# Performance work log

Hardware: AMD Instinct MI355X
Metric: run time of the kernel (lower is better)

The kernel has to match this reference:

```python
import jax, jax.numpy as jnp
import numpy as np

B, T, D_MODEL, N_HEADS, HEAD = 2, 2048, 1024, 16, 64
ROPE_BASE = 10000.0
EPS = 1e-5


def _layer_norm(x, g, b):
    m = jnp.mean(x, axis=-1, keepdims=True)
    v = jnp.var(x, axis=-1, keepdims=True)
    return (x - m) * jax.lax.rsqrt(v + EPS) * g + b


def _rope(x):
    # x: [B, H, T, D]; interleaved-pair rotary embedding along T
    d = x.shape[-1]
    t = x.shape[-2]
    theta = 1.0 / (ROPE_BASE ** (jnp.arange(0, d, 2, dtype=jnp.float32) / d))  # [D/2]
    ang = jnp.arange(t, dtype=jnp.float32)[:, None] * theta[None, :]  # [T, D/2]
    cos = jnp.cos(ang)[None, None, :, :]
    sin = jnp.sin(ang)[None, None, :, :]
    x1 = x[..., 0::2]
    x2 = x[..., 1::2]
    out = jnp.stack([x1 * cos - x2 * sin, x1 * sin + x2 * cos], axis=-1)
    return out.reshape(x.shape)


def setup_inputs() -> dict:
    key = jax.random.key(0)
    ks = jax.random.split(key, 12)
    sc = 0.02
    x = jax.random.normal(ks[0], (B, T, D_MODEL), jnp.float32)
    # key-padding mask: last 128 key positions masked out
    mask = (jnp.arange(T) < T - 128).astype(jnp.int32)
    mask = jnp.broadcast_to(mask[None, None, None, :], (B, 1, T, T))
    return {
        "x": x,
        "mask": mask,
        "wq": jax.random.normal(ks[1], (D_MODEL, D_MODEL), jnp.float32) * sc,
        "wk": jax.random.normal(ks[2], (D_MODEL, D_MODEL), jnp.float32) * sc,
        "wv": jax.random.normal(ks[3], (D_MODEL, D_MODEL), jnp.float32) * sc,
        "w_proj": jax.random.normal(ks[4], (D_MODEL, D_MODEL), jnp.float32) * sc,
        "b_proj": jnp.zeros((D_MODEL,), jnp.float32),
        "ln1_g": jnp.ones((D_MODEL,), jnp.float32),
        "ln1_b": jnp.zeros((D_MODEL,), jnp.float32),
        "ln2_g": jnp.ones((D_MODEL,), jnp.float32),
        "ln2_b": jnp.zeros((D_MODEL,), jnp.float32),
        "w1": jax.random.normal(ks[5], (D_MODEL, 4 * D_MODEL), jnp.float32) * sc,
        "b1": jnp.zeros((4 * D_MODEL,), jnp.float32),
        "w2": jax.random.normal(ks[6], (4 * D_MODEL, D_MODEL), jnp.float32) * sc,
        "b2": jnp.zeros((D_MODEL,), jnp.float32),
    }


def reference(x, mask, wq, wk, wv, w_proj, b_proj, ln1_g, ln1_b, ln2_g, ln2_b, w1, b1, w2, b2):
    Bx, Tx, D = x.shape
    # --- self-attention with pre-norm ---
    h = _layer_norm(x, ln1_g, ln1_b)
    q = (h @ wq).reshape(Bx, Tx, N_HEADS, HEAD).transpose(0, 2, 1, 3)  # [B,H,T,d]
    k = (h @ wk).reshape(Bx, Tx, N_HEADS, HEAD).transpose(0, 2, 1, 3)
    v = (h @ wv).reshape(Bx, Tx, N_HEADS, HEAD).transpose(0, 2, 1, 3)
    q = _rope(q)
    k = _rope(k)
    scores = jnp.einsum("bhtd,bhsd->bhts", q, k) * (HEAD ** -0.5)
    scores = jnp.where(mask == 0, -jnp.inf, scores)
    w = jax.nn.softmax(scores, axis=-1)
    att = jnp.einsum("bhts,bhsd->bhtd", w, v)
    att = att.transpose(0, 2, 1, 3).reshape(Bx, Tx, D)
    x = x + att @ w_proj + b_proj
    # --- feed-forward with pre-norm ---
    h2 = _layer_norm(x, ln2_g, ln2_b)
    x = x + jax.nn.relu(h2 @ w1 + b1) @ w2 + b2
    return x
```

## Files before the change

### kernel.cpp

```cpp
#include <hip/hip_runtime.h>
#include <hip/hip_bf16.h>
#include <math.h>

#define TT 2048
#define NKV 30

typedef __attribute__((ext_vector_type(8))) short bf16x8;
typedef __attribute__((ext_vector_type(4))) float f32x4;
typedef __attribute__((ext_vector_type(16))) float f32x16;
typedef __hip_bfloat16 bf16;

__device__ __forceinline__ short f2bf(float f) {
  bf16 h = __float2bfloat16(f);
  return *(short*)&h;
}
__device__ __forceinline__ float bf2f(short s) {
  union { unsigned u; float f; } x; x.u = ((unsigned)(unsigned short)s) << 16; return x.f;
}

__device__ __forceinline__ void gload_lds16(const void* g, void* l) {
  __builtin_amdgcn_global_load_lds(
      (const __attribute__((address_space(1))) void*)g,
      (__attribute__((address_space(3))) void*)l, 16, 0, 0);
}

__device__ __forceinline__ unsigned cvt_pk_bf16(float lo, float hi) {
  unsigned r;
  asm("v_cvt_pk_bf16_f32 %0, %1, %2" : "=v"(r) : "v"(lo), "v"(hi));
  return r;
}

__global__ __launch_bounds__(256) void k_transpose(const float* __restrict__ in,
                                                   bf16* __restrict__ out, int R, int C) {
  __shared__ float tile[32][33];
  int bc = blockIdx.x * 32, br = blockIdx.y * 32;
  int tx = threadIdx.x & 31, ty = threadIdx.x >> 5;
#pragma unroll
  for (int i = 0; i < 32; i += 8)
    tile[ty + i][tx] = in[(size_t)(br + ty + i) * C + bc + tx];
  __syncthreads();
#pragma unroll
  for (int i = 0; i < 32; i += 8)
    out[(size_t)(bc + ty + i) * R + br + tx] = __float2bfloat16(tile[tx][ty + i]);
}

__global__ __launch_bounds__(256) void k_layernorm(const float* __restrict__ x,
                                                   const float* __restrict__ g,
                                                   const float* __restrict__ bb,
                                                   bf16* __restrict__ out) {
  int row = blockIdx.x, t = threadIdx.x;
  const float4* xr = (const float4*)(x + (size_t)row * 1024);
  float4 v = xr[t];
  float s = v.x + v.y + v.z + v.w;
  float ss = v.x * v.x + v.y * v.y + v.z * v.z + v.w * v.w;
#pragma unroll
  for (int off = 32; off > 0; off >>= 1) { s += __shfl_xor(s, off); ss += __shfl_xor(ss, off); }
  __shared__ float red[8];
  int w = t >> 6;
  if ((t & 63) == 0) { red[w] = s; red[4 + w] = ss; }
  __syncthreads();
  s = red[0] + red[1] + red[2] + red[3];
  ss = red[4] + red[5] + red[6] + red[7];
  float mean = s * (1.f / 1024.f);
  float var = ss * (1.f / 1024.f) - mean * mean;
  float rs = rsqrtf(var + 1e-5f);
  float4 gv = ((const float4*)g)[t], bv = ((const float4*)bb)[t];
  short4 o;
  o.x = f2bf((v.x - mean) * rs * gv.x + bv.x);
  o.y = f2bf((v.y - mean) * rs * gv.y + bv.y);
  o.z = f2bf((v.z - mean) * rs * gv.z + bv.z);
  o.w = f2bf((v.w - mean) * rs * gv.w + bv.w);
  *(short4*)((short*)out + (size_t)row * 1024 + t * 4) = o;
}

__global__ __launch_bounds__(256) void k_rope_table(float2* __restrict__ cs) {
  int idx = blockIdx.x * 256 + threadIdx.x;
  int t = idx >> 5, i = idx & 31;
  float theta = powf(10000.f, -(float)(2 * i) / 64.f);
  float sv, cv;
  sincosf((float)t * theta, &sv, &cv);
  cs[idx] = make_float2(cv, sv);
}

__global__ __launch_bounds__(256) void k_rope_apply(bf16* __restrict__ q, bf16* __restrict__ k,
                                                    const float2* __restrict__ cs) {
  int idx = blockIdx.x * 256 + threadIdx.x;
  bf16* base = (idx >> 21) ? k : q;
  int rem = idx & ((1 << 21) - 1);
  int bht = rem >> 5, i = rem & 31;
  int t = bht & (TT - 1);
  float2 c = cs[(t << 5) + i];
  short* p = (short*)base + ((size_t)bht << 6) + 2 * i;
  unsigned pv = *(unsigned*)p;
  float x1 = bf2f((short)(pv & 0xffff)), x2 = bf2f((short)(pv >> 16));
  short o1 = f2bf(x1 * c.x - x2 * c.y);
  short o2 = f2bf(x1 * c.y + x2 * c.x);
  *(unsigned*)p = ((unsigned)(unsigned short)o1) | (((unsigned)(unsigned short)o2) << 16);
}

__global__ __launch_bounds__(256) void k_add(float* __restrict__ out,
                                             const float* __restrict__ part) {
  size_t i = (size_t)blockIdx.x * 256 + threadIdx.x;
  float4 a = ((const float4*)out)[i];
  float4 b = ((const float4*)part)[i];
  a.x += b.x; a.y += b.y; a.z += b.z; a.w += b.w;
  ((float4*)out)[i] = a;
}

template <int EPI>
__global__ __launch_bounds__(256) void k_gemm(const bf16* __restrict__ A,
                                              const bf16* __restrict__ Bt,
                                              void* __restrict__ out,
                                              const float* __restrict__ bias,
                                              const float* __restrict__ add,
                                              void* __restrict__ out2,
                                              int M, int N, int K) {
  __shared__ char a_lds[2][8192];
  __shared__ char b_lds[2][8192];
  int t = threadIdx.x, l = t & 63, w = t >> 6;
  int lane16 = l & 15, lg = l >> 4;
  int m0 = blockIdx.y << 7, n0 = blockIdx.x << 7;
  int wr = w >> 1, wc = w & 1;
  f32x4 acc[4][4] = {};
  const int kslice = K / gridDim.z;
  const int kb0 = blockIdx.z * kslice;
  const short* Ap = (const short*)A + (size_t)(m0 + (t >> 2)) * K + kb0 + (t & 3) * 8;
  const short* Bp = (const short*)Bt + (size_t)(n0 + (t >> 2)) * K + kb0 + (t & 3) * 8;
  size_t rowskip = (size_t)64 * K;
  const int nk = kslice >> 5;

  auto stage = [&](int buf, int k0) {
    gload_lds16(Ap + k0, &a_lds[buf][t * 16]);
    gload_lds16(Ap + rowskip + k0, &a_lds[buf][4096 + t * 16]);
    gload_lds16(Bp + k0, &b_lds[buf][t * 16]);
    gload_lds16(Bp + rowskip + k0, &b_lds[buf][4096 + t * 16]);
  };
  stage(0, 0);
  __syncthreads();
  for (int ki = 0; ki < nk; ++ki) {
    const int cur = ki & 1;
    if (ki + 1 < nk) stage(cur ^ 1, (ki + 1) << 5);
    bf16x8 af[4], bfr[4];
#pragma unroll
    for (int mi = 0; mi < 4; ++mi)
      af[mi] = *(const bf16x8*)(&a_lds[cur][(wr * 64 + mi * 16 + lane16) * 64 + lg * 16]);
#pragma unroll
    for (int ni = 0; ni < 4; ++ni)
      bfr[ni] = *(const bf16x8*)(&b_lds[cur][(wc * 64 + ni * 16 + lane16) * 64 + lg * 16]);
#pragma unroll
    for (int mi = 0; mi < 4; ++mi)
#pragma unroll
      for (int ni = 0; ni < 4; ++ni)
        acc[mi][ni] = __builtin_amdgcn_mfma_f32_16x16x32_bf16(af[mi], bfr[ni], acc[mi][ni], 0, 0, 0);
    if (ki + 1 < nk) __syncthreads();
  }
#pragma unroll
  for (int mi = 0; mi < 4; ++mi) {
#pragma unroll
    for (int ni = 0; ni < 4; ++ni) {
      int row0 = m0 + wr * 64 + mi * 16 + lg * 4;
      int col = n0 + wc * 64 + ni * 16 + lane16;
      if (EPI == 0) {
        int which = col >> 10, f = col & 1023;
        int hh = f >> 6, d = f & 63;
        int bb = row0 >> 11, tk = row0 & (TT - 1);
        if (which == 2) {
          short4 o;
          o.x = f2bf(acc[mi][ni][0]); o.y = f2bf(acc[mi][ni][1]);
          o.z = f2bf(acc[mi][ni][2]); o.w = f2bf(acc[mi][ni][3]);
          *(short4*)((short*)out2 + ((size_t)((bb * 16 + hh) * 64 + d)) * TT + tk) = o;
        } else {
#pragma unroll
          for (int i = 0; i < 4; ++i)
            ((bf16*)out)[(size_t)which * 4194304 +
                         ((size_t)((bb * 16 + hh) * TT + tk + i)) * 64 + d] =
                __float2bfloat16(acc[mi][ni][i]);
        }
      } else if (EPI == 1) {
#pragma unroll
        for (int i = 0; i < 4; ++i)
          ((float*)out)[(size_t)(row0 + i) * N + col] =
              acc[mi][ni][i] + bias[col] + add[(size_t)(row0 + i) * N + col];
      } else if (EPI == 2) {
#pragma unroll
        for (int i = 0; i < 4; ++i) {
          float r2 = acc[mi][ni][i] + bias[col];
          ((bf16*)out)[(size_t)(row0 + i) * N + col] = __float2bfloat16(r2 > 0.f ? r2 : 0.f);
        }
      } else {
        if (blockIdx.z == 0) {
#pragma unroll
          for (int i = 0; i < 4; ++i)
            ((float*)out)[(size_t)(row0 + i) * N + col] =
                acc[mi][ni][i] + bias[col] + add[(size_t)(row0 + i) * N + col];
        } else {
#pragma unroll
          for (int i = 0; i < 4; ++i)
            ((float*)out2)[(size_t)(row0 + i) * N + col] = acc[mi][ni][i];
        }
      }
    }
  }
}

__global__ __launch_bounds__(512) void k_attn(const bf16* __restrict__ qb,
                                              const bf16* __restrict__ kb,
                                              const bf16* __restrict__ vt,
                                              bf16* __restrict__ att) {
  __shared__ char lds[2][16384];
  const int t = threadIdx.x, l = t & 63, w = t >> 6;
  const int q31 = l & 31, hi = l >> 5;
  const int bh = blockIdx.y, qblk = blockIdx.x;
  const int b = bh >> 4, hh = bh & 15;

  const int qrow = qblk * 256 + w * 32 + q31;
  const short* qp = (const short*)qb + ((size_t)bh * TT + qrow) * 64 + hi * 8;
  bf16x8 qf[4];
#pragma unroll
  for (int s = 0; s < 4; ++s) qf[s] = *(const bf16x8*)(qp + s * 16);

  const int srow = t >> 3, sch = (t & 7) ^ (srow & 7);
  const short* kgp = (const short*)kb + (size_t)bh * TT * 64 + (size_t)srow * 64 + sch * 8;
  const short* vgp = (const short*)vt + (size_t)bh * 64 * TT + (size_t)srow * TT + sch * 8;

  float m_i = -INFINITY, l_i = 0.f;
  f32x16 oacc0 = {}, oacc1 = {};

  gload_lds16(kgp, &lds[0][t * 16]);
  gload_lds16(vgp, &lds[0][8192 + t * 16]);
  __syncthreads();

  for (int kt = 0; kt < NKV; ++kt) {
    const int cur = kt & 1;
    if (kt + 1 < NKV) {
      gload_lds16(kgp + (size_t)(kt + 1) * 64 * 64, &lds[cur ^ 1][t * 16]);
      gload_lds16(vgp + (kt + 1) * 64, &lds[cur ^ 1][8192 + t * 16]);
    }
    const char* kl = lds[cur];
    const char* vl = lds[cur] + 8192;

    f32x16 sacc[2] = {};
    __builtin_amdgcn_s_setprio(1);
#pragma unroll
    for (int kb2 = 0; kb2 < 2; ++kb2) {
      const int krow = kb2 * 32 + q31;
      const char* krp = kl + krow * 128;
      const int sw = krow & 7;
#pragma unroll
      for (int s = 0; s < 4; ++s) {
        bf16x8 kf = *(const bf16x8*)(krp + (((s * 2 + hi) ^ sw) * 16));
        sacc[kb2] = __builtin_amdgcn_mfma_f32_32x32x16_bf16(kf, qf[s], sacc[kb2], 0, 0, 0);
      }
    }
    __builtin_amdgcn_s_setprio(0);

    float pm = -INFINITY;
#pragma unroll
    for (int kb2 = 0; kb2 < 2; ++kb2)
#pragma unroll
      for (int r = 0; r < 16; ++r) pm = fmaxf(pm, sacc[kb2][r]);
    pm = fmaxf(pm, __shfl_xor(pm, 32));
    pm *= 0.125f;
    if (!__all(pm <= m_i + 8.f)) {
      float mnew = fmaxf(m_i, pm);
      float corr = __expf(m_i - mnew);
      m_i = mnew;
      l_i *= corr;
#pragma unroll
      for (int r = 0; r < 16; ++r) {
        float cq = __shfl(corr, (r & 3) + 8 * (r >> 2) + 4 * hi);
        oacc0[r] *= cq;
        oacc1[r] *= cq;
      }
    }
    float psum = 0.f;
#pragma unroll
    for (int kb2 = 0; kb2 < 2; ++kb2)
#pragma unroll
      for (int r = 0; r < 16; ++r) {
        float p = __expf(sacc[kb2][r] * 0.125f - m_i);
        sacc[kb2][r] = p;
        psum += p;
      }
    psum += __shfl_xor(psum, 32);
    l_i += psum;

    bf16x8 pfrag[4];
#pragma unroll
    for (int kb2 = 0; kb2 < 2; ++kb2)
#pragma unroll
      for (int ks = 0; ks < 2; ++ks) {
        unsigned A0 = cvt_pk_bf16(sacc[kb2][8 * ks + 0], sacc[kb2][8 * ks + 1]);
        unsigned A1 = cvt_pk_bf16(sacc[kb2][8 * ks + 2], sacc[kb2][8 * ks + 3]);
        unsigned B0 = cvt_pk_bf16(sacc[kb2][8 * ks + 4], sacc[kb2][8 * ks + 5]);
        unsigned B1 = cvt_pk_bf16(sacc[kb2][8 * ks + 6], sacc[kb2][8 * ks + 7]);
        auto s0 = __builtin_amdgcn_permlane32_swap(A0, B0, false, false);
        auto s1 = __builtin_amdgcn_permlane32_swap(A1, B1, false, false);
        union { unsigned w4[4]; bf16x8 v; } u;
        u.w4[0] = s0[0]; u.w4[1] = s1[0]; u.w4[2] = s0[1]; u.w4[3] = s1[1];
        pfrag[kb2 * 2 + ks] = u.v;
      }

    {
      const char* vr0 = vl + q31 * 128;
      const char* vr1 = vl + (32 + q31) * 128;
      const int sw = q31 & 7;
      __builtin_amdgcn_s_setprio(1);
#pragma unroll
      for (int gs = 0; gs < 4; ++gs) {
        bf16x8 v0 = *(const bf16x8*)(vr0 + (((gs * 2 + hi) ^ sw) * 16));
        bf16x8 v1 = *(const bf16x8*)(vr1 + (((gs * 2 + hi) ^ sw) * 16));
        oacc0 = __builtin_amdgcn_mfma_f32_32x32x16_bf16(pfrag[gs], v0, oacc0, 0, 0, 0);
        oacc1 = __builtin_amdgcn_mfma_f32_32x32x16_bf16(pfrag[gs], v1, oacc1, 0, 0, 0);
      }
      __builtin_amdgcn_s_setprio(0);
    }
    __syncthreads();
  }

  float inv = 1.f / l_i;
#pragma unroll
  for (int r = 0; r < 16; ++r) {
    const int qr = (r & 3) + 8 * (r >> 2) + 4 * hi;
    float invq = __shfl(inv, qr);
    size_t base = ((size_t)(b * TT + qblk * 256 + w * 32 + qr)) * 1024 + hh * 64 + q31;
    att[base] = __float2bfloat16(oacc0[r] * invq);
    att[base + 32] = __float2bfloat16(oacc1[r] * invq);
  }
}

extern "C" void kernel_launch(void* const* d_in, const int* in_sizes, int n_in,
                              void* d_out, int out_size, void* d_ws, size_t ws_size,
                              hipStream_t stream) {
  const float* x      = (const float*)d_in[0];
  const float* wq     = (const float*)d_in[2];
  const float* wk     = (const float*)d_in[3];
  const float* wv     = (const float*)d_in[4];
  const float* w_proj = (const float*)d_in[5];
  const float* b_proj = (const float*)d_in[6];
  const float* ln1_g  = (const float*)d_in[7];
  const float* ln1_b  = (const float*)d_in[8];
  const float* ln2_g  = (const float*)d_in[9];
  const float* ln2_b  = (const float*)d_in[10];
  const float* w1     = (const float*)d_in[11];
  const float* b1     = (const float*)d_in[12];
  const float* w2     = (const float*)d_in[13];
  const float* b2     = (const float*)d_in[14];
  float* out = (float*)d_out;

  char* ws = (char*)d_ws;
  size_t off = 0;
  auto alloc = [&](size_t bytes) {
    char* p = ws + off;
    off += (bytes + 255) & ~(size_t)255;
    return p;
  };
  float2* cs   = (float2*)alloc((size_t)TT * 32 * sizeof(float2));
  bf16* h      = (bf16*)alloc((size_t)4096 * 1024 * 2);
  bf16* wqkvT  = (bf16*)alloc((size_t)3072 * 1024 * 2);
  bf16* wprojT = (bf16*)alloc((size_t)1024 * 1024 * 2);
  bf16* w1T    = (bf16*)alloc((size_t)4096 * 1024 * 2);
  bf16* w2T    = (bf16*)alloc((size_t)1024 * 4096 * 2);
  bf16* qkv    = (bf16*)alloc((size_t)2 * 4194304 * 2);
  bf16* vtb    = (bf16*)alloc((size_t)4194304 * 2);
  bf16* attb   = (bf16*)alloc((size_t)4096 * 1024 * 2);
  float* x2    = (float*)alloc((size_t)4096 * 1024 * 4);
  bf16* h2     = (bf16*)alloc((size_t)4096 * 1024 * 2);
  bf16* gbuf   = qkv;
  float* mlp2p = (float*)h;

  k_rope_table<<<dim3(256), dim3(256), 0, stream>>>(cs);
  k_transpose<<<dim3(32, 32), dim3(256), 0, stream>>>(wq, wqkvT, 1024, 1024);
  k_transpose<<<dim3(32, 32), dim3(256), 0, stream>>>(wk, wqkvT + 1024 * 1024, 1024, 1024);
  k_transpose<<<dim3(32, 32), dim3(256), 0, stream>>>(wv, wqkvT + 2 * 1024 * 1024, 1024, 1024);
  k_transpose<<<dim3(32, 32), dim3(256), 0, stream>>>(w_proj, wprojT, 1024, 1024);
  k_transpose<<<dim3(128, 32), dim3(256), 0, stream>>>(w1, w1T, 1024, 4096);
  k_transpose<<<dim3(32, 128), dim3(256), 0, stream>>>(w2, w2T, 4096, 1024);
  k_layernorm<<<dim3(4096), dim3(256), 0, stream>>>(x, ln1_g, ln1_b, h);
  k_gemm<0><<<dim3(24, 32), dim3(256), 0, stream>>>(h, wqkvT, (void*)qkv, nullptr, nullptr,
                                                    (void*)vtb, 4096, 3072, 1024);
  k_rope_apply<<<dim3(16384), dim3(256), 0, stream>>>(qkv, qkv + 4194304, cs);
  k_attn<<<dim3(8, 32), dim3(512), 0, stream>>>(qkv, qkv + 4194304, vtb, attb);
  k_gemm<1><<<dim3(8, 32), dim3(256), 0, stream>>>(attb, wprojT, (void*)x2, b_proj, x,
                                                   nullptr, 4096, 1024, 1024);
  k_layernorm<<<dim3(4096), dim3(256), 0, stream>>>(x2, ln2_g, ln2_b, h2);
  k_gemm<2><<<dim3(32, 32), dim3(256), 0, stream>>>(h2, w1T, (void*)gbuf, b1, nullptr,
                                                    nullptr, 4096, 4096, 1024);
  k_gemm<3><<<dim3(8, 32, 2), dim3(256), 0, stream>>>(gbuf, w2T, (void*)out, b2, x2,
                                                      (void*)mlp2p, 4096, 1024, 4096);
  k_add<<<dim3(4096), dim3(256), 0, stream>>>(out, mlp2p);
}
```

Before: 396.3 us.

## Add 256x256 pipelined GEMM kernel for QKV and MLP with 4-way split-K

Adds a new 512-thread GEMM with 256x256 tiles, a 128KB LDS multi-stage pipeline, swizzled LDS addressing, explicit vmcnt waits and barriers, and an XCD-aware block remap. The QKV, MLP-up and MLP-down GEMMs now use it. MLP-down becomes a 4-way split-K whose partials are stored as bf16 into reused buffers and summed by a three-input add kernel. The aim is more data reuse per tile and better overlap of loads with MFMA. The risks are lower occupancy (one block per CU), fewer blocks for the smaller GEMMs, and precision loss from bf16 partial sums.

After: 377.1 us. -4.8%, faster.

```diff
diff --git a/kernel.cpp b/kernel.cpp
--- a/kernel.cpp
+++ b/kernel.cpp
@@ -98,12 +98,19 @@
   *(unsigned*)p = ((unsigned)(unsigned short)o1) | (((unsigned)(unsigned short)o2) << 16);
 }
 
-__global__ __launch_bounds__(256) void k_add(float* __restrict__ out,
-                                             const float* __restrict__ part) {
+__global__ __launch_bounds__(256) void k_add3(float* __restrict__ out,
+                                              const bf16* __restrict__ p1,
+                                              const bf16* __restrict__ p2,
+                                              const bf16* __restrict__ p3) {
   size_t i = (size_t)blockIdx.x * 256 + threadIdx.x;
   float4 a = ((const float4*)out)[i];
-  float4 b = ((const float4*)part)[i];
-  a.x += b.x; a.y += b.y; a.z += b.z; a.w += b.w;
+  short4 b1 = ((const short4*)p1)[i];
+  short4 b2 = ((const short4*)p2)[i];
+  short4 b3 = ((const short4*)p3)[i];
+  a.x += bf2f(b1.x) + bf2f(b2.x) + bf2f(b3.x);
+  a.y += bf2f(b1.y) + bf2f(b2.y) + bf2f(b3.y);
+  a.z += bf2f(b1.z) + bf2f(b2.z) + bf2f(b3.z);
+  a.w += bf2f(b1.w) + bf2f(b2.w) + bf2f(b3.w);
   ((float4*)out)[i] = a;
 }
 
@@ -122,12 +129,10 @@
   int m0 = blockIdx.y << 7, n0 = blockIdx.x << 7;
   int wr = w >> 1, wc = w & 1;
   f32x4 acc[4][4] = {};
-  const int kslice = K / gridDim.z;
-  const int kb0 = blockIdx.z * kslice;
-  const short* Ap = (const short*)A + (size_t)(m0 + (t >> 2)) * K + kb0 + (t & 3) * 8;
-  const short* Bp = (const short*)Bt + (size_t)(n0 + (t >> 2)) * K + kb0 + (t & 3) * 8;
+  const short* Ap = (const short*)A + (size_t)(m0 + (t >> 2)) * K + (t & 3) * 8;
+  const short* Bp = (const short*)Bt + (size_t)(n0 + (t >> 2)) * K + (t & 3) * 8;
   size_t rowskip = (size_t)64 * K;
-  const int nk = kslice >> 5;
+  const int nk = K >> 5;
 
   auto stage = [&](int buf, int k0) {
     gload_lds16(Ap + k0, &a_lds[buf][t * 16]);
@@ -160,31 +165,136 @@
     for (int ni = 0; ni < 4; ++ni) {
       int row0 = m0 + wr * 64 + mi * 16 + lg * 4;
       int col = n0 + wc * 64 + ni * 16 + lane16;
+#pragma unroll
+      for (int i = 0; i < 4; ++i)
+        ((float*)out)[(size_t)(row0 + i) * N + col] =
+            acc[mi][ni][i] + bias[col] + add[(size_t)(row0 + i) * N + col];
+    }
+  }
+}
+
+#define VM8 asm volatile("s_waitcnt vmcnt(8)" ::: "memory")
+#define VM4 asm volatile("s_waitcnt vmcnt(4)" ::: "memory")
+#define VM0 asm volatile("s_waitcnt vmcnt(0)" ::: "memory")
+#define VMX
+
+#define STAGE_A(BUF, J, H)                                                              \
+  gload_lds16(Ag0 + (J) * 64 + (H) * 32, lds + (BUF) * 32768 + (H) * 16384 + t * 16);   \
+  gload_lds16(Ag1 + (J) * 64 + (H) * 32, lds + (BUF) * 32768 + (H) * 16384 + 8192 + t * 16)
+
+#define STAGE_B(BUF, J, H)                                                                      \
+  gload_lds16(Bg0 + (J) * 64 + (H) * 32, lds + 65536 + (BUF) * 32768 + (H) * 16384 + t * 16);   \
+  gload_lds16(Bg1 + (J) * 64 + (H) * 32, lds + 65536 + (BUF) * 32768 + (H) * 16384 + 8192 + t * 16)
+
+#define PHASE(BUF, H, QM, STG, WAIT)                                                          \
+  {                                                                                           \
+    const char* ab_ = lds + (BUF) * 32768 + (H) * 16384;                                      \
+    if ((QM) == 0) {                                                                          \
+      bfr[0] = *(const bf16x8*)(ab_ + boff);                                                  \
+      bfr[1] = *(const bf16x8*)(ab_ + boff + 1024);                                           \
+      bfr[2] = *(const bf16x8*)(ab_ + boff + 2048);                                           \
+      bfr[3] = *(const bf16x8*)(ab_ + boff + 3072);                                           \
+    }                                                                                         \
+    afr[0] = *(const bf16x8*)(ab_ + aoff + (QM) * 4096);                                      \
+    afr[1] = *(const bf16x8*)(ab_ + aoff + (QM) * 4096 + 1024);                               \
+    afr[2] = *(const bf16x8*)(ab_ + aoff + (QM) * 4096 + 2048);                               \
+    afr[3] = *(const bf16x8*)(ab_ + aoff + (QM) * 4096 + 3072);                               \
+    STG;                                                                                      \
+    __builtin_amdgcn_s_barrier();                                                             \
+    asm volatile("s_waitcnt lgkmcnt(0)" ::: "memory");                                        \
+    __builtin_amdgcn_sched_barrier(0);                                                        \
+    __builtin_amdgcn_s_setprio(1);                                                            \
+    _Pragma("unroll") for (int mm_ = 0; mm_ < 4; ++mm_)                                       \
+        _Pragma("unroll") for (int nn_ = 0; nn_ < 4; ++nn_)                                   \
+            acc[(QM) * 4 + mm_][nn_] = __builtin_amdgcn_mfma_f32_16x16x32_bf16(               \
+                afr[mm_], bfr[nn_], acc[(QM) * 4 + mm_][nn_], 0, 0, 0);                       \
+    __builtin_amdgcn_s_setprio(0);                                                            \
+    WAIT;                                                                                     \
+    __builtin_amdgcn_s_barrier();                                                             \
+  }
+
+#define KTILE(BUF, J, S01, S23, WMID, WEND)                       \
+  PHASE(BUF, 0, 0, { if (S01) { STAGE_A((BUF) ^ 1, (J) + 1, 1); } }, VMX); \
+  PHASE(BUF, 0, 1, { if (S01) { STAGE_B((BUF) ^ 1, (J) + 1, 1); } }, WMID); \
+  PHASE(BUF, 1, 0, { if (S23) { STAGE_A((BUF), (J) + 2, 0); } }, VMX);      \
+  PHASE(BUF, 1, 1, { if (S23) { STAGE_B((BUF), (J) + 2, 0); } }, WEND)
+
+template <int EPI>
+__global__ __launch_bounds__(512, 1) void k_gemm256(const bf16* __restrict__ A,
+                                                    const bf16* __restrict__ Bt,
+                                                    void* __restrict__ out,
+                                                    const float* __restrict__ bias,
+                                                    const float* __restrict__ add,
+                                                    void* __restrict__ out2,
+                                                    bf16* __restrict__ p1,
+                                                    bf16* __restrict__ p2,
+                                                    bf16* __restrict__ p3,
+                                                    int N, int K) {
+  __shared__ char lds[131072];
+  const int t = threadIdx.x, l = t & 63, w = t >> 6;
+  const int lane16 = l & 15, lg = l >> 4;
+  const int wr = w >> 2, wc = w & 3;
+  int flat = blockIdx.y * gridDim.x + blockIdx.x;
+  const int nwg = gridDim.x * gridDim.y;
+  flat = (flat & 7) * (nwg >> 3) + (flat >> 3);
+  const int bx = flat % gridDim.x, by = flat / gridDim.x;
+  const int m0 = by << 8, n0 = bx << 8;
+  const int kb0 = blockIdx.z << 10;
+
+  const int tq = t >> 2;
+  const int clog = (t & 3) ^ ((t >> 4) & 3);
+  const short* Ag0 = (const short*)A + (size_t)(m0 + tq) * K + kb0 + clog * 8;
+  const short* Ag1 = Ag0 + (size_t)128 * K;
+  const short* Bg0 = (const short*)Bt + (size_t)(n0 + tq) * K + kb0 + clog * 8;
+  const short* Bg1 = Bg0 + (size_t)128 * K;
+
+  const int sw16 = ((l >> 4) ^ ((l >> 2) & 3)) * 16;
+  const int aoff = (wr * 128 + lane16) * 64 + sw16;
+  const int boff = 65536 + (wc * 64 + lane16) * 64 + sw16;
+
+  f32x4 acc[8][4] = {};
+  bf16x8 afr[4], bfr[4];
+
+  STAGE_A(0, 0, 0); STAGE_B(0, 0, 0);
+  STAGE_A(0, 0, 1); STAGE_B(0, 0, 1);
+  STAGE_A(1, 1, 0); STAGE_B(1, 1, 0);
+  VM8;
+  __builtin_amdgcn_s_barrier();
+
+  for (int jj = 0; jj < 7; ++jj) {
+    const int j0 = jj * 2;
+    KTILE(0, j0, true, true, VM8, VM8);
+    KTILE(1, j0 + 1, true, true, VM8, VM8);
+  }
+  KTILE(0, 14, true, false, VM8, VM4);
+  KTILE(1, 15, false, false, VM0, VMX);
+
+#pragma unroll
+  for (int mi = 0; mi < 8; ++mi) {
+#pragma unroll
+    for (int ni = 0; ni < 4; ++ni) {
+      int row0 = m0 + wr * 128 + mi * 16 + lg * 4;
+      int col = n0 + wc * 64 + ni * 16 + lane16;
+      f32x4 a = acc[mi][ni];
       if (EPI == 0) {
         int which = col >> 10, f = col & 1023;
         int hh = f >> 6, d = f & 63;
         int bb = row0 >> 11, tk = row0 & (TT - 1);
         if (which == 2) {
           short4 o;
-          o.x = f2bf(acc[mi][ni][0]); o.y = f2bf(acc[mi][ni][1]);
-          o.z = f2bf(acc[mi][ni][2]); o.w = f2bf(acc[mi][ni][3]);
+          o.x = f2bf(a[0]); o.y = f2bf(a[1]); o.z = f2bf(a[2]); o.w = f2bf(a[3]);
           *(short4*)((short*)out2 + ((size_t)((bb * 16 + hh) * 64 + d)) * TT + tk) = o;
         } else {
 #pragma unroll
           for (int i = 0; i < 4; ++i)
             ((bf16*)out)[(size_t)which * 4194304 +
                          ((size_t)((bb * 16 + hh) * TT + tk + i)) * 64 + d] =
-                __float2bfloat16(acc[mi][ni][i]);
+                __float2bfloat16(a[i]);
         }
-      } else if (EPI == 1) {
-#pragma unroll
-        for (int i = 0; i < 4; ++i)
-          ((float*)out)[(size_t)(row0 + i) * N + col] =
-              acc[mi][ni][i] + bias[col] + add[(size_t)(row0 + i) * N + col];
       } else if (EPI == 2) {
 #pragma unroll
         for (int i = 0; i < 4; ++i) {
-          float r2 = acc[mi][ni][i] + bias[col];
+          float r2 = a[i] + bias[col];
           ((bf16*)out)[(size_t)(row0 + i) * N + col] = __float2bfloat16(r2 > 0.f ? r2 : 0.f);
         }
       } else {
@@ -192,11 +302,12 @@
 #pragma unroll
           for (int i = 0; i < 4; ++i)
             ((float*)out)[(size_t)(row0 + i) * N + col] =
-                acc[mi][ni][i] + bias[col] + add[(size_t)(row0 + i) * N + col];
+                a[i] + bias[col] + add[(size_t)(row0 + i) * N + col];
         } else {
+          bf16* pp = blockIdx.z == 1 ? p1 : (blockIdx.z == 2 ? p2 : p3);
 #pragma unroll
           for (int i = 0; i < 4; ++i)
-            ((float*)out2)[(size_t)(row0 + i) * N + col] = acc[mi][ni][i];
+            pp[(size_t)(row0 + i) * N + col] = __float2bfloat16(a[i]);
         }
       }
     }
@@ -367,7 +478,9 @@
   float* x2    = (float*)alloc((size_t)4096 * 1024 * 4);
   bf16* h2     = (bf16*)alloc((size_t)4096 * 1024 * 2);
   bf16* gbuf   = qkv;
-  float* mlp2p = (float*)h;
+  bf16* mp1 = h;
+  bf16* mp2 = w1T;
+  bf16* mp3 = h2;
 
   k_rope_table<<<dim3(256), dim3(256), 0, stream>>>(cs);
   k_transpose<<<dim3(32, 32), dim3(256), 0, stream>>>(wq, wqkvT, 1024, 1024);
@@ -377,16 +490,19 @@
   k_transpose<<<dim3(128, 32), dim3(256), 0, stream>>>(w1, w1T, 1024, 4096);
   k_transpose<<<dim3(32, 128), dim3(256), 0, stream>>>(w2, w2T, 4096, 1024);
   k_layernorm<<<dim3(4096), dim3(256), 0, stream>>>(x, ln1_g, ln1_b, h);
-  k_gemm<0><<<dim3(24, 32), dim3(256), 0, stream>>>(h, wqkvT, (void*)qkv, nullptr, nullptr,
-                                                    (void*)vtb, 4096, 3072, 1024);
+  k_gemm256<0><<<dim3(12, 16), dim3(512), 0, stream>>>(h, wqkvT, (void*)qkv, nullptr, nullptr,
+                                                       (void*)vtb, nullptr, nullptr, nullptr,
+                                                       3072, 1024);
   k_rope_apply<<<dim3(16384), dim3(256), 0, stream>>>(qkv, qkv + 4194304, cs);
   k_attn<<<dim3(8, 32), dim3(512), 0, stream>>>(qkv, qkv + 4194304, vtb, attb);
   k_gemm<1><<<dim3(8, 32), dim3(256), 0, stream>>>(attb, wprojT, (void*)x2, b_proj, x,
                                                    nullptr, 4096, 1024, 1024);
   k_layernorm<<<dim3(4096), dim3(256), 0, stream>>>(x2, ln2_g, ln2_b, h2);
-  k_gemm<2><<<dim3(32, 32), dim3(256), 0, stream>>>(h2, w1T, (void*)gbuf, b1, nullptr,
-                                                    nullptr, 4096, 4096, 1024);
-  k_gemm<3><<<dim3(8, 32, 2), dim3(256), 0, stream>>>(gbuf, w2T, (void*)out, b2, x2,
-                                                      (void*)mlp2p, 4096, 1024, 4096);
-  k_add<<<dim3(4096), dim3(256), 0, stream>>>(out, mlp2p);
-}
+  k_gemm256<2><<<dim3(16, 16), dim3(512), 0, stream>>>(h2, w1T, (void*)gbuf, b1, nullptr,
+                                                       nullptr, nullptr, nullptr, nullptr,
+                                                       4096, 1024);
+  k_gemm256<3><<<dim3(4, 16, 4), dim3(512), 0, stream>>>(gbuf, w2T, (void*)out, b2, x2,
+                                                         nullptr, mp1, mp2, mp3,
+                                                         1024, 4096);
+  k_add3<<<dim3(4096), dim3(256), 0, stream>>>(out, mp1, mp2, mp3);
+}
```
